# Kernel optimization log

Hardware: AMD Instinct MI355X
Metric: run time of the kernel (lower is better)

The kernel has to match this reference:

```python
import jax, jax.numpy as jnp
import numpy as np


def setup_inputs() -> dict:
    key = jax.random.key(0)
    k1, k2, k3, k4, k5 = jax.random.split(key, 5)
    b, t_q, t_k = 4, 256, 1024
    qs, ms, n = 512, 512, 128
    return {
        "query": jax.random.normal(k1, (b, t_q, qs), dtype=jnp.float32),
        "keys": jax.random.normal(k2, (b, t_k, ms), dtype=jnp.float32),
        "Wq": jax.random.normal(k3, (qs, n), dtype=jnp.float32) * 0.05,
        "Wk": jax.random.normal(k4, (ms, n), dtype=jnp.float32) * 0.05,
        "linear_att": jax.random.normal(k5, (n,), dtype=jnp.float32) * 0.05,
    }


def reference(query, keys, Wq, Wk, linear_att):
    # projections: b t_q n and b t_k n
    att_query = jnp.einsum("bqd,dn->bqn", query, Wq)
    att_keys = jnp.einsum("bkd,dn->bkn", keys, Wk)
    # Bahdanau additive score: tanh(q + k) . v  -> b t_q t_k
    sum_qk = att_query[:, :, None, :] + att_keys[:, None, :, :]
    scores = jnp.einsum("bqkn,n->bqk", jnp.tanh(sum_qk), linear_att)
    weights = jax.nn.softmax(scores, axis=-1)
    context = jnp.einsum("bqk,bkd->bqd", weights, keys)
    return (context, weights)
```

## Files before the change

### kernel.cpp

```cpp
#include <hip/hip_runtime.h>

#define B 4
#define TQ 256
#define TK 1024
#define QS 512
#define NN 128

#define TANH_SCALE 2.8853900817779268f
#define LOG2E 1.4426950408889634f
#define CTX_ELEMS ((size_t)B * TQ * QS)

__device__ __forceinline__ float fast_exp2(float x) {
#if __has_builtin(__builtin_amdgcn_exp2f)
    return __builtin_amdgcn_exp2f(x);
#else
    return exp2f(x);
#endif
}
__device__ __forceinline__ float fast_rcp(float x) {
#if __has_builtin(__builtin_amdgcn_rcpf)
    return __builtin_amdgcn_rcpf(x);
#else
    return 1.0f / x;
#endif
}

__global__ __launch_bounds__(64) void proj_kernel(
    const float* __restrict__ query, const float* __restrict__ keys,
    const float* __restrict__ Wq, const float* __restrict__ Wk,
    float* __restrict__ attq, float* __restrict__ attkT)
{
    __shared__ float As[32][12];
    __shared__ float Bs[32][132];

    const int tid = threadIdx.x;
    const int rb = blockIdx.x * 8;
    const bool isq = (rb < B * TQ);
    const float* A = isq ? (query + (size_t)rb * QS)
                         : (keys + (size_t)(rb - B * TQ) * QS);
    const float* W = isq ? Wq : Wk;

    const int n0 = (tid & 31) * 4;
    const int q0 = (tid >> 5) * 4;
    float acc[4][4] = {};

    for (int k0 = 0; k0 < QS; k0 += 32) {
        {
            const int r = tid >> 3, c4 = tid & 7;
            const float4 v = *(const float4*)(A + (size_t)r * QS + k0 + c4 * 4);
            As[c4 * 4 + 0][r] = v.x;
            As[c4 * 4 + 1][r] = v.y;
            As[c4 * 4 + 2][r] = v.z;
            As[c4 * 4 + 3][r] = v.w;
        }
        {
            const int n4 = (tid & 31) * 4, kg = tid >> 5;
            #pragma unroll
            for (int j = 0; j < 16; ++j) {
                const int kk = kg + j * 2;
                *(float4*)&Bs[kk][n4] =
                    *(const float4*)(W + (size_t)(k0 + kk) * NN + n4);
            }
        }
        __syncthreads();
        #pragma unroll
        for (int kk = 0; kk < 32; ++kk) {
            const float4 a = *(const float4*)&As[kk][q0];
            const float4 b = *(const float4*)&Bs[kk][n0];
            const float av[4] = {a.x, a.y, a.z, a.w};
            #pragma unroll
            for (int i = 0; i < 4; ++i) {
                acc[i][0] = fmaf(av[i], b.x, acc[i][0]);
                acc[i][1] = fmaf(av[i], b.y, acc[i][1]);
                acc[i][2] = fmaf(av[i], b.z, acc[i][2]);
                acc[i][3] = fmaf(av[i], b.w, acc[i][3]);
            }
        }
        __syncthreads();
    }

    if (isq) {
        #pragma unroll
        for (int i = 0; i < 4; ++i) {
            float4 o;
            o.x = fast_exp2(acc[i][0] * TANH_SCALE);
            o.y = fast_exp2(acc[i][1] * TANH_SCALE);
            o.z = fast_exp2(acc[i][2] * TANH_SCALE);
            o.w = fast_exp2(acc[i][3] * TANH_SCALE);
            *(float4*)(attq + (size_t)(rb + q0 + i) * NN + n0) = o;
        }
    } else {
        #pragma unroll
        for (int i = 0; i < 4; ++i) {
            float4 o;
            o.x = fast_exp2(acc[i][0] * TANH_SCALE);
            o.y = fast_exp2(acc[i][1] * TANH_SCALE);
            o.z = fast_exp2(acc[i][2] * TANH_SCALE);
            o.w = fast_exp2(acc[i][3] * TANH_SCALE);
            *(float4*)&Bs[q0 + i][n0] = o;
        }
        __syncthreads();
        const int rk = rb - B * TQ;
        const int bb = rk >> 10;
        const int kbase = rk & 1023;
        #pragma unroll
        for (int h = 0; h < 2; ++h) {
            const int n = tid + h * 64;
            float* o = attkT + (size_t)bb * NN * TK + (size_t)n * TK + kbase;
            float4 t0, t1;
            t0.x = Bs[0][n]; t0.y = Bs[1][n]; t0.z = Bs[2][n]; t0.w = Bs[3][n];
            t1.x = Bs[4][n]; t1.y = Bs[5][n]; t1.z = Bs[6][n]; t1.w = Bs[7][n];
            *(float4*)(o + 0) = t0;
            *(float4*)(o + 4) = t1;
        }
    }
}

__global__ __launch_bounds__(256) void score_softmax_kernel(
    const float* __restrict__ attq, const float* __restrict__ attkT,
    const float* __restrict__ vatt, float* __restrict__ wout)
{
    __shared__ float eqs[2][128];
    __shared__ float nv2[128];
    __shared__ float red[2][8];

    const int tid = threadIdx.x;
    const int b = blockIdx.x >> 7;
    const int q0 = (blockIdx.x & 127) * 2;

    if (tid < 128) {
        eqs[0][tid] = attq[((size_t)b * TQ + q0) * NN + tid];
        nv2[tid] = -2.0f * vatt[tid];
    } else {
        eqs[1][tid & 127] = attq[((size_t)b * TQ + q0 + 1) * NN + (tid & 127)];
    }
    __syncthreads();

    const float* kt = attkT + (size_t)b * NN * TK + (size_t)tid * 4;
    float s[2][4] = {};

    #pragma unroll 8
    for (int n = 0; n < 128; ++n) {
        const float4 a = *(const float4*)(kt + (size_t)n * TK);
        const float e0 = eqs[0][n], e1 = eqs[1][n], nv = nv2[n];
        const float av[4] = {a.x, a.y, a.z, a.w};
        #pragma unroll
        for (int rr = 0; rr < 4; ++rr) {
            const float r0 = fast_rcp(fmaf(av[rr], e0, 1.0f));
            s[0][rr] = fmaf(nv, r0, s[0][rr]);
            const float r1 = fast_rcp(fmaf(av[rr], e1, 1.0f));
            s[1][rr] = fmaf(nv, r1, s[1][rr]);
        }
    }

    const int lane = tid & 63, wid = tid >> 6;
    #pragma unroll
    for (int qq = 0; qq < 2; ++qq) {
        float mm = fmaxf(fmaxf(s[qq][0], s[qq][1]), fmaxf(s[qq][2], s[qq][3]));
        #pragma unroll
        for (int off = 32; off > 0; off >>= 1)
            mm = fmaxf(mm, __shfl_xor(mm, off, 64));
        if (lane == 0) red[qq][wid] = mm;
    }
    __syncthreads();
    float m[2];
    m[0] = fmaxf(fmaxf(red[0][0], red[0][1]), fmaxf(red[0][2], red[0][3]));
    m[1] = fmaxf(fmaxf(red[1][0], red[1][1]), fmaxf(red[1][2], red[1][3]));

    float e[2][4];
    #pragma unroll
    for (int qq = 0; qq < 2; ++qq) {
        float ls = 0.f;
        #pragma unroll
        for (int i = 0; i < 4; ++i) {
            e[qq][i] = fast_exp2((s[qq][i] - m[qq]) * LOG2E);
            ls += e[qq][i];
        }
        #pragma unroll
        for (int off = 32; off > 0; off >>= 1)
            ls += __shfl_xor(ls, off, 64);
        if (lane == 0) red[qq][4 + wid] = ls;
    }
    __syncthreads();
    #pragma unroll
    for (int qq = 0; qq < 2; ++qq) {
        const float S = red[qq][4] + red[qq][5] + red[qq][6] + red[qq][7];
        const float inv = fast_rcp(S);
        float4 w4;
        w4.x = e[qq][0] * inv; w4.y = e[qq][1] * inv;
        w4.z = e[qq][2] * inv; w4.w = e[qq][3] * inv;
        *(float4*)(wout + ((size_t)b * TQ + q0 + qq) * TK + (size_t)tid * 4) = w4;
    }
}

__global__ __launch_bounds__(256) void context_kernel(
    const float* __restrict__ keys, const float* __restrict__ w,
    float* __restrict__ ctxp)
{
    __shared__ float Wst[32][66];
    __shared__ float Ks[32][64];

    const int tid = threadIdx.x;
    const int bid = blockIdx.x;
    const int b = bid >> 7;
    const int rem = bid & 127;
    const int qt = rem >> 5;
    const int dt = (rem >> 2) & 7;
    const int ks = rem & 3;

    const float* wb = w + (size_t)b * TQ * TK + (size_t)qt * 64 * TK + ks * 256;
    const float* kb = keys + (size_t)b * TK * QS + (size_t)ks * 256 * QS + dt * 64;

    const int d0 = (tid & 15) * 4;
    const int q0 = (tid >> 4) * 4;
    float acc[4][4] = {};

    const int wr = tid >> 2;
    const int wc = (tid & 3) * 8;

    for (int k0 = 0; k0 < 256; k0 += 32) {
        {
            const float4 v0 = *(const float4*)(wb + (size_t)wr * TK + k0 + wc);
            const float4 v1 = *(const float4*)(wb + (size_t)wr * TK + k0 + wc + 4);
            Wst[wc + 0][wr] = v0.x; Wst[wc + 1][wr] = v0.y;
            Wst[wc + 2][wr] = v0.z; Wst[wc + 3][wr] = v0.w;
            Wst[wc + 4][wr] = v1.x; Wst[wc + 5][wr] = v1.y;
            Wst[wc + 6][wr] = v1.z; Wst[wc + 7][wr] = v1.w;
        }
        {
            const int c = tid & 15, rr = tid >> 4;
            *(float4*)&Ks[rr][c * 4] =
                *(const float4*)(kb + (size_t)(k0 + rr) * QS + c * 4);
            *(float4*)&Ks[rr + 16][c * 4] =
                *(const float4*)(kb + (size_t)(k0 + rr + 16) * QS + c * 4);
        }
        __syncthreads();
        #pragma unroll
        for (int kk = 0; kk < 32; ++kk) {
            const float2 a01 = *(const float2*)&Wst[kk][q0];
            const float2 a23 = *(const float2*)&Wst[kk][q0 + 2];
            const float4 bb = *(const float4*)&Ks[kk][d0];
            const float av[4] = {a01.x, a01.y, a23.x, a23.y};
            #pragma unroll
            for (int i = 0; i < 4; ++i) {
                acc[i][0] = fmaf(av[i], bb.x, acc[i][0]);
                acc[i][1] = fmaf(av[i], bb.y, acc[i][1]);
                acc[i][2] = fmaf(av[i], bb.z, acc[i][2]);
                acc[i][3] = fmaf(av[i], bb.w, acc[i][3]);
            }
        }
        __syncthreads();
    }

    float* op = ctxp + (size_t)ks * CTX_ELEMS
              + ((size_t)b * TQ + qt * 64 + q0) * QS + dt * 64 + d0;
    #pragma unroll
    for (int i = 0; i < 4; ++i) {
        float4 o;
        o.x = acc[i][0]; o.y = acc[i][1]; o.z = acc[i][2]; o.w = acc[i][3];
        *(float4*)(op + (size_t)i * QS) = o;
    }
}

__global__ __launch_bounds__(256) void reduce_kernel(
    const float4* __restrict__ ctxp, float4* __restrict__ ctx)
{
    const size_t idx = (size_t)blockIdx.x * 256 + threadIdx.x;
    const size_t stride = CTX_ELEMS / 4;
    const float4 a = ctxp[idx];
    const float4 b = ctxp[idx + stride];
    const float4 c = ctxp[idx + 2 * stride];
    const float4 d = ctxp[idx + 3 * stride];
    float4 o;
    o.x = (a.x + b.x) + (c.x + d.x);
    o.y = (a.y + b.y) + (c.y + d.y);
    o.z = (a.z + b.z) + (c.z + d.z);
    o.w = (a.w + b.w) + (c.w + d.w);
    ctx[idx] = o;
}

extern "C" void kernel_launch(void* const* d_in, const int* in_sizes, int n_in,
                              void* d_out, int out_size, void* d_ws, size_t ws_size,
                              hipStream_t stream) {
    const float* query = (const float*)d_in[0];
    const float* keys  = (const float*)d_in[1];
    const float* Wq    = (const float*)d_in[2];
    const float* Wk    = (const float*)d_in[3];
    const float* vatt  = (const float*)d_in[4];

    float* ctx = (float*)d_out;
    float* wts = ctx + CTX_ELEMS;

    float* attq  = (float*)d_ws;
    float* attkT = attq + (size_t)B * TQ * NN;
    float* ctxp  = attkT + (size_t)B * NN * TK;

    hipLaunchKernelGGL(proj_kernel, dim3((B * TQ + B * TK) / 8), dim3(64), 0,
                       stream, query, keys, Wq, Wk, attq, attkT);
    hipLaunchKernelGGL(score_softmax_kernel, dim3(B * TQ / 2), dim3(256), 0,
                       stream, attq, attkT, vatt, wts);
    hipLaunchKernelGGL(context_kernel, dim3(512), dim3(256), 0,
                       stream, keys, wts, ctxp);
    hipLaunchKernelGGL(reduce_kernel, dim3((unsigned)(CTX_ELEMS / 4 / 256)), dim3(256), 0,
                       stream, (const float4*)ctxp, (float4*)ctx);
}
```

Baseline: 137.0 us.

## Use split-bf16 MFMA for projection and context GEMMs

Replaces the FP32 FMA projection and context GEMMs with MFMA 16x16x32 bf16 kernels. Each fp32 operand is split into hi and lo bf16 parts and accumulated with three MFMAs to approximate fp32 accuracy. A new transpose/split kernel pre-converts keys and weights into transposed bf16 hi/lo buffers. This adds an extra launch and extra memory traffic and workspace, and accuracy is slightly below full fp32.

```diff
diff --git a/kernel.cpp b/kernel.cpp
--- a/kernel.cpp
+++ b/kernel.cpp
@@ -9,6 +9,12 @@
 #define TANH_SCALE 2.8853900817779268f
 #define LOG2E 1.4426950408889634f
 #define CTX_ELEMS ((size_t)B * TQ * QS)
+
+typedef unsigned short ushort_t;
+typedef __attribute__((ext_vector_type(8))) short bfrag;
+typedef __attribute__((ext_vector_type(4))) float ffrag;
+
+union FragU { uint4 u; bfrag s; };
 
 __device__ __forceinline__ float fast_exp2(float x) {
 #if __has_builtin(__builtin_amdgcn_exp2f)
@@ -25,93 +31,146 @@
 #endif
 }
 
-__global__ __launch_bounds__(64) void proj_kernel(
+__device__ __forceinline__ unsigned int pk_bf16(float a, float b) {
+    unsigned int r;
+    asm("v_cvt_pk_bf16_f32 %0, %1, %2" : "=v"(r) : "v"(a), "v"(b));
+    return r;
+}
+__device__ __forceinline__ float lo16f(unsigned int u) { return __uint_as_float(u << 16); }
+__device__ __forceinline__ float hi16f(unsigned int u) { return __uint_as_float(u & 0xffff0000u); }
+
+__device__ __forceinline__ void split_frag(float4 a0, float4 a1, FragU& hi, FragU& lo) {
+    const unsigned int h0 = pk_bf16(a0.x, a0.y), h1 = pk_bf16(a0.z, a0.w);
+    const unsigned int h2 = pk_bf16(a1.x, a1.y), h3 = pk_bf16(a1.z, a1.w);
+    const float l0 = a0.x - lo16f(h0), l1 = a0.y - hi16f(h0);
+    const float l2 = a0.z - lo16f(h1), l3 = a0.w - hi16f(h1);
+    const float l4 = a1.x - lo16f(h2), l5 = a1.y - hi16f(h2);
+    const float l6 = a1.z - lo16f(h3), l7 = a1.w - hi16f(h3);
+    hi.u = make_uint4(h0, h1, h2, h3);
+    lo.u = make_uint4(pk_bf16(l0, l1), pk_bf16(l2, l3),
+                      pk_bf16(l4, l5), pk_bf16(l6, l7));
+}
+
+__global__ __launch_bounds__(256) void transpose_split_kernel(
+    const float* __restrict__ keys, const float* __restrict__ Wq,
+    const float* __restrict__ Wk,
+    ushort_t* __restrict__ keysT_hi, ushort_t* __restrict__ keysT_lo,
+    ushort_t* __restrict__ WT_hi, ushort_t* __restrict__ WT_lo)
+{
+    __shared__ float t[32][33];
+    const int tid = threadIdx.x;
+    const int bid = blockIdx.x;
+    const float* src; ushort_t *dh, *dl;
+    int srcLD, dstLD, r0, c0;
+    if (bid < 2048) {
+        const int b = bid >> 9, tt = bid & 511;
+        const int kt = tt & 31, dt = tt >> 5;
+        src = keys + (size_t)b * TK * QS; srcLD = QS;
+        dh = keysT_hi + (size_t)b * QS * TK;
+        dl = keysT_lo + (size_t)b * QS * TK;
+        dstLD = TK; r0 = kt * 32; c0 = dt * 32;
+    } else {
+        const int tt = bid - 2048;
+        const int m = tt >> 6, t2 = tt & 63;
+        const int kt = t2 & 15, nt = t2 >> 4;
+        src = m ? Wk : Wq; srcLD = NN;
+        dh = WT_hi + (size_t)m * NN * QS;
+        dl = WT_lo + (size_t)m * NN * QS;
+        dstLD = QS; r0 = kt * 32; c0 = nt * 32;
+    }
+    {
+        const int rr = tid >> 3, cc = (tid & 7) * 4;
+        const float4 v = *(const float4*)(src + (size_t)(r0 + rr) * srcLD + c0 + cc);
+        t[rr][cc + 0] = v.x; t[rr][cc + 1] = v.y;
+        t[rr][cc + 2] = v.z; t[rr][cc + 3] = v.w;
+    }
+    __syncthreads();
+    {
+        const int dr = tid >> 3, kc = (tid & 7) * 4;
+        const float v0 = t[kc + 0][dr], v1 = t[kc + 1][dr];
+        const float v2 = t[kc + 2][dr], v3 = t[kc + 3][dr];
+        const unsigned int h01 = pk_bf16(v0, v1), h23 = pk_bf16(v2, v3);
+        const float l0 = v0 - lo16f(h01), l1 = v1 - hi16f(h01);
+        const float l2 = v2 - lo16f(h23), l3 = v3 - hi16f(h23);
+        const unsigned int L01 = pk_bf16(l0, l1), L23 = pk_bf16(l2, l3);
+        const size_t o = (size_t)(c0 + dr) * dstLD + r0 + kc;
+        uint2 h; h.x = h01; h.y = h23;
+        uint2 L; L.x = L01; L.y = L23;
+        *(uint2*)(dh + o) = h;
+        *(uint2*)(dl + o) = L;
+    }
+}
+
+__global__ __launch_bounds__(256) void proj_mfma_kernel(
     const float* __restrict__ query, const float* __restrict__ keys,
-    const float* __restrict__ Wq, const float* __restrict__ Wk,
+    const ushort_t* __restrict__ WT_hi, const ushort_t* __restrict__ WT_lo,
     float* __restrict__ attq, float* __restrict__ attkT)
 {
-    __shared__ float As[32][12];
-    __shared__ float Bs[32][132];
-
-    const int tid = threadIdx.x;
-    const int rb = blockIdx.x * 8;
-    const bool isq = (rb < B * TQ);
-    const float* A = isq ? (query + (size_t)rb * QS)
-                         : (keys + (size_t)(rb - B * TQ) * QS);
-    const float* W = isq ? Wq : Wk;
-
-    const int n0 = (tid & 31) * 4;
-    const int q0 = (tid >> 5) * 4;
-    float acc[4][4] = {};
-
-    for (int k0 = 0; k0 < QS; k0 += 32) {
-        {
-            const int r = tid >> 3, c4 = tid & 7;
-            const float4 v = *(const float4*)(A + (size_t)r * QS + k0 + c4 * 4);
-            As[c4 * 4 + 0][r] = v.x;
-            As[c4 * 4 + 1][r] = v.y;
-            As[c4 * 4 + 2][r] = v.z;
-            As[c4 * 4 + 3][r] = v.w;
-        }
-        {
-            const int n4 = (tid & 31) * 4, kg = tid >> 5;
+    __shared__ float As[4][16][36];
+    const int tid = threadIdx.x, lane = tid & 63, w = tid >> 6;
+    const int r0 = blockIdx.x * 32;
+    const bool isq = (r0 < B * TQ);
+    const float* Abase = isq ? (query + (size_t)r0 * QS)
+                             : (keys + (size_t)(r0 - B * TQ) * QS);
+    const ushort_t* BH = WT_hi + (isq ? 0 : (size_t)NN * QS);
+    const ushort_t* BL = WT_lo + (isq ? 0 : (size_t)NN * QS);
+    const int rb = w >> 1;
+    const int nb0 = (w & 1) * 64;
+    const int frow = lane & 15, fg = lane >> 4;
+    const float* Arow = Abase + (size_t)(rb * 16) * QS;
+
+    ffrag acc[4] = {};
+    #pragma unroll 2
+    for (int kb = 0; kb < QS; kb += 32) {
+        FragU bh[4], bl[4];
+        #pragma unroll
+        for (int nb = 0; nb < 4; ++nb) {
+            const size_t off = (size_t)(nb0 + nb * 16 + frow) * QS + kb + fg * 8;
+            bh[nb].u = *(const uint4*)(BH + off);
+            bl[nb].u = *(const uint4*)(BL + off);
+        }
+        #pragma unroll
+        for (int it = 0; it < 2; ++it) {
+            const int f = lane + it * 64;
+            const int rr = f >> 3, cc = f & 7;
+            *(float4*)&As[w][rr][cc * 4] =
+                *(const float4*)(Arow + (size_t)rr * QS + kb + cc * 4);
+        }
+        const float4 a0 = *(const float4*)&As[w][frow][fg * 8];
+        const float4 a1 = *(const float4*)&As[w][frow][fg * 8 + 4];
+        FragU ah, al;
+        split_frag(a0, a1, ah, al);
+        #pragma unroll
+        for (int nb = 0; nb < 4; ++nb) {
+            acc[nb] = __builtin_amdgcn_mfma_f32_16x16x32_bf16(al.s, bh[nb].s, acc[nb], 0, 0, 0);
+            acc[nb] = __builtin_amdgcn_mfma_f32_16x16x32_bf16(ah.s, bl[nb].s, acc[nb], 0, 0, 0);
+            acc[nb] = __builtin_amdgcn_mfma_f32_16x16x32_bf16(ah.s, bh[nb].s, acc[nb], 0, 0, 0);
+        }
+    }
+
+    const int orow = rb * 16 + fg * 4;
+    if (isq) {
+        #pragma unroll
+        for (int nb = 0; nb < 4; ++nb) {
+            const int n = nb0 + nb * 16 + frow;
             #pragma unroll
-            for (int j = 0; j < 16; ++j) {
-                const int kk = kg + j * 2;
-                *(float4*)&Bs[kk][n4] =
-                    *(const float4*)(W + (size_t)(k0 + kk) * NN + n4);
-            }
-        }
-        __syncthreads();
-        #pragma unroll
-        for (int kk = 0; kk < 32; ++kk) {
-            const float4 a = *(const float4*)&As[kk][q0];
-            const float4 b = *(const float4*)&Bs[kk][n0];
-            const float av[4] = {a.x, a.y, a.z, a.w};
-            #pragma unroll
-            for (int i = 0; i < 4; ++i) {
-                acc[i][0] = fmaf(av[i], b.x, acc[i][0]);
-                acc[i][1] = fmaf(av[i], b.y, acc[i][1]);
-                acc[i][2] = fmaf(av[i], b.z, acc[i][2]);
-                acc[i][3] = fmaf(av[i], b.w, acc[i][3]);
-            }
-        }
-        __syncthreads();
-    }
-
-    if (isq) {
-        #pragma unroll
-        for (int i = 0; i < 4; ++i) {
+            for (int r = 0; r < 4; ++r)
+                attq[(size_t)(r0 + orow + r) * NN + n] =
+                    fast_exp2(acc[nb][r] * TANH_SCALE);
+        }
+    } else {
+        const int rk = r0 - B * TQ;
+        const int bb = rk >> 10;
+        const int kk = (rk & 1023) + orow;
+        #pragma unroll
+        for (int nb = 0; nb < 4; ++nb) {
+            const int n = nb0 + nb * 16 + frow;
             float4 o;
-            o.x = fast_exp2(acc[i][0] * TANH_SCALE);
-            o.y = fast_exp2(acc[i][1] * TANH_SCALE);
-            o.z = fast_exp2(acc[i][2] * TANH_SCALE);
-            o.w = fast_exp2(acc[i][3] * TANH_SCALE);
-            *(float4*)(attq + (size_t)(rb + q0 + i) * NN + n0) = o;
-        }
-    } else {
-        #pragma unroll
-        for (int i = 0; i < 4; ++i) {
-            float4 o;
-            o.x = fast_exp2(acc[i][0] * TANH_SCALE);
-            o.y = fast_exp2(acc[i][1] * TANH_SCALE);
-            o.z = fast_exp2(acc[i][2] * TANH_SCALE);
-            o.w = fast_exp2(acc[i][3] * TANH_SCALE);
-            *(float4*)&Bs[q0 + i][n0] = o;
-        }
-        __syncthreads();
-        const int rk = rb - B * TQ;
-        const int bb = rk >> 10;
-        const int kbase = rk & 1023;
-        #pragma unroll
-        for (int h = 0; h < 2; ++h) {
-            const int n = tid + h * 64;
-            float* o = attkT + (size_t)bb * NN * TK + (size_t)n * TK + kbase;
-            float4 t0, t1;
-            t0.x = Bs[0][n]; t0.y = Bs[1][n]; t0.z = Bs[2][n]; t0.w = Bs[3][n];
-            t1.x = Bs[4][n]; t1.y = Bs[5][n]; t1.z = Bs[6][n]; t1.w = Bs[7][n];
-            *(float4*)(o + 0) = t0;
-            *(float4*)(o + 4) = t1;
+            o.x = fast_exp2(acc[nb][0] * TANH_SCALE);
+            o.y = fast_exp2(acc[nb][1] * TANH_SCALE);
+            o.z = fast_exp2(acc[nb][2] * TANH_SCALE);
+            o.w = fast_exp2(acc[nb][3] * TANH_SCALE);
+            *(float4*)(attkT + (size_t)bb * NN * TK + (size_t)n * TK + kk) = o;
         }
     }
 }
@@ -193,72 +252,58 @@
     }
 }
 
-__global__ __launch_bounds__(256) void context_kernel(
-    const float* __restrict__ keys, const float* __restrict__ w,
-    float* __restrict__ ctxp)
-{
-    __shared__ float Wst[32][66];
-    __shared__ float Ks[32][64];
-
-    const int tid = threadIdx.x;
+__global__ __launch_bounds__(256) void context_mfma_kernel(
+    const float* __restrict__ wts, const ushort_t* __restrict__ KTh,
+    const ushort_t* __restrict__ KTl, float* __restrict__ ctxp)
+{
+    __shared__ float As[4][16][36];
+    const int tid = threadIdx.x, lane = tid & 63, w = tid >> 6;
     const int bid = blockIdx.x;
-    const int b = bid >> 7;
-    const int rem = bid & 127;
-    const int qt = rem >> 5;
-    const int dt = (rem >> 2) & 7;
-    const int ks = rem & 3;
-
-    const float* wb = w + (size_t)b * TQ * TK + (size_t)qt * 64 * TK + ks * 256;
-    const float* kb = keys + (size_t)b * TK * QS + (size_t)ks * 256 * QS + dt * 64;
-
-    const int d0 = (tid & 15) * 4;
-    const int q0 = (tid >> 4) * 4;
-    float acc[4][4] = {};
-
-    const int wr = tid >> 2;
-    const int wc = (tid & 3) * 8;
-
-    for (int k0 = 0; k0 < 256; k0 += 32) {
-        {
-            const float4 v0 = *(const float4*)(wb + (size_t)wr * TK + k0 + wc);
-            const float4 v1 = *(const float4*)(wb + (size_t)wr * TK + k0 + wc + 4);
-            Wst[wc + 0][wr] = v0.x; Wst[wc + 1][wr] = v0.y;
-            Wst[wc + 2][wr] = v0.z; Wst[wc + 3][wr] = v0.w;
-            Wst[wc + 4][wr] = v1.x; Wst[wc + 5][wr] = v1.y;
-            Wst[wc + 6][wr] = v1.z; Wst[wc + 7][wr] = v1.w;
-        }
-        {
-            const int c = tid & 15, rr = tid >> 4;
-            *(float4*)&Ks[rr][c * 4] =
-                *(const float4*)(kb + (size_t)(k0 + rr) * QS + c * 4);
-            *(float4*)&Ks[rr + 16][c * 4] =
-                *(const float4*)(kb + (size_t)(k0 + rr + 16) * QS + c * 4);
-        }
-        __syncthreads();
-        #pragma unroll
-        for (int kk = 0; kk < 32; ++kk) {
-            const float2 a01 = *(const float2*)&Wst[kk][q0];
-            const float2 a23 = *(const float2*)&Wst[kk][q0 + 2];
-            const float4 bb = *(const float4*)&Ks[kk][d0];
-            const float av[4] = {a01.x, a01.y, a23.x, a23.y};
-            #pragma unroll
-            for (int i = 0; i < 4; ++i) {
-                acc[i][0] = fmaf(av[i], bb.x, acc[i][0]);
-                acc[i][1] = fmaf(av[i], bb.y, acc[i][1]);
-                acc[i][2] = fmaf(av[i], bb.z, acc[i][2]);
-                acc[i][3] = fmaf(av[i], bb.w, acc[i][3]);
-            }
-        }
-        __syncthreads();
-    }
-
+    const int ks = bid & 3, dt = (bid >> 2) & 3;
+    const int qt = (bid >> 4) & 7, b = bid >> 7;
+    const int rb = w >> 1, nb0 = (w & 1) * 64;
+    const int frow = lane & 15, fg = lane >> 4;
+
+    const float* Arow = wts + ((size_t)b * TQ + qt * 32 + rb * 16) * TK + ks * 256;
+    const ushort_t* BH = KTh + ((size_t)b * QS + dt * 128) * TK + ks * 256;
+    const ushort_t* BL = KTl + ((size_t)b * QS + dt * 128) * TK + ks * 256;
+
+    ffrag acc[4] = {};
+    #pragma unroll 2
+    for (int kb = 0; kb < 256; kb += 32) {
+        FragU bh[4], bl[4];
+        #pragma unroll
+        for (int nb = 0; nb < 4; ++nb) {
+            const size_t off = (size_t)(nb0 + nb * 16 + frow) * TK + kb + fg * 8;
+            bh[nb].u = *(const uint4*)(BH + off);
+            bl[nb].u = *(const uint4*)(BL + off);
+        }
+        #pragma unroll
+        for (int it = 0; it < 2; ++it) {
+            const int f = lane + it * 64, rr = f >> 3, cc = f & 7;
+            *(float4*)&As[w][rr][cc * 4] =
+                *(const float4*)(Arow + (size_t)rr * TK + kb + cc * 4);
+        }
+        const float4 a0 = *(const float4*)&As[w][frow][fg * 8];
+        const float4 a1 = *(const float4*)&As[w][frow][fg * 8 + 4];
+        FragU ah, al;
+        split_frag(a0, a1, ah, al);
+        #pragma unroll
+        for (int nb = 0; nb < 4; ++nb) {
+            acc[nb] = __builtin_amdgcn_mfma_f32_16x16x32_bf16(al.s, bh[nb].s, acc[nb], 0, 0, 0);
+            acc[nb] = __builtin_amdgcn_mfma_f32_16x16x32_bf16(ah.s, bl[nb].s, acc[nb], 0, 0, 0);
+            acc[nb] = __builtin_amdgcn_mfma_f32_16x16x32_bf16(ah.s, bh[nb].s, acc[nb], 0, 0, 0);
+        }
+    }
+
+    const int qrow = qt * 32 + rb * 16 + fg * 4;
     float* op = ctxp + (size_t)ks * CTX_ELEMS
-              + ((size_t)b * TQ + qt * 64 + q0) * QS + dt * 64 + d0;
+              + ((size_t)b * TQ + qrow) * QS + dt * 128 + nb0 + frow;
     #pragma unroll
-    for (int i = 0; i < 4; ++i) {
-        float4 o;
-        o.x = acc[i][0]; o.y = acc[i][1]; o.z = acc[i][2]; o.w = acc[i][3];
-        *(float4*)(op + (size_t)i * QS) = o;
+    for (int nb = 0; nb < 4; ++nb) {
+        #pragma unroll
+        for (int r = 0; r < 4; ++r)
+            op[(size_t)r * QS + nb * 16] = acc[nb][r];
     }
 }
 
@@ -294,13 +339,19 @@
     float* attq  = (float*)d_ws;
     float* attkT = attq + (size_t)B * TQ * NN;
     float* ctxp  = attkT + (size_t)B * NN * TK;
-
-    hipLaunchKernelGGL(proj_kernel, dim3((B * TQ + B * TK) / 8), dim3(64), 0,
-                       stream, query, keys, Wq, Wk, attq, attkT);
+    ushort_t* keysT_hi = (ushort_t*)(ctxp + 4 * CTX_ELEMS);
+    ushort_t* keysT_lo = keysT_hi + (size_t)B * QS * TK;
+    ushort_t* WT_hi    = keysT_lo + (size_t)B * QS * TK;
+    ushort_t* WT_lo    = WT_hi + (size_t)2 * NN * QS;
+
+    hipLaunchKernelGGL(transpose_split_kernel, dim3(2176), dim3(256), 0, stream,
+                       keys, Wq, Wk, keysT_hi, keysT_lo, WT_hi, WT_lo);
+    hipLaunchKernelGGL(proj_mfma_kernel, dim3(160), dim3(256), 0, stream,
+                       query, keys, WT_hi, WT_lo, attq, attkT);
     hipLaunchKernelGGL(score_softmax_kernel, dim3(B * TQ / 2), dim3(256), 0,
                        stream, attq, attkT, vatt, wts);
-    hipLaunchKernelGGL(context_kernel, dim3(512), dim3(256), 0,
-                       stream, keys, wts, ctxp);
+    hipLaunchKernelGGL(context_mfma_kernel, dim3(512), dim3(256), 0, stream,
+                       wts, keysT_hi, keysT_lo, ctxp);
     hipLaunchKernelGGL(reduce_kernel, dim3((unsigned)(CTX_ELEMS / 4 / 256)), dim3(256), 0,
                        stream, (const float4*)ctxp, (float4*)ctx);
 }
```

New measurement: 137.7 us. About the same (+0.5%).
